# Optimization experiments

Measured on AMD Instinct MI355X. Metric: run time of the kernel, lower is better.

## Reference

```python
import jax, jax.numpy as jnp
import numpy as np

EPSILON = 1e-15
CUTOFF = 5.0
N_RBF = 16           # num_radial_filters -> RBF dim = 2*16+1 = 33
SCALE = 8            # _quadrature_points_per_atom_scaling


def poly_envelope_5_2(x):
    # e3nn.poly_envelope(5, 2): f'(x) ~ x^5 (1-x)^2, f(0)=1, f(1)=0
    x2 = x * x
    x6 = x2 * x2 * x2
    f = 1.0 - 28.0 * x6 + 48.0 * x6 * x - 21.0 * x6 * x2
    return jnp.where(x < 1.0, f, jnp.zeros_like(x))


def sin_cos_basis(r, n_rbf):
    r = r[..., None]                                  # [A,T,1]
    k = jnp.arange(1, n_rbf + 1, dtype=r.dtype)       # [n_rbf]
    return jnp.sqrt(2.0) * jnp.concatenate(
        [0.1 * jnp.ones_like(r), jnp.sin(k * jnp.pi * r), jnp.cos(k * jnp.pi * r)],
        axis=-1,
    )                                                 # [A,T,2*n_rbf+1]


def spherical_harmonics_l012_norm(d):
    # Real spherical harmonics up to l=2, e3nn m-ordering, normalization='norm'
    # (each l-block has unit norm for unit input directions).
    x, y, z = d[..., 0], d[..., 1], d[..., 2]
    r2 = x * x + y * y + z * z
    s3 = jnp.sqrt(3.0)
    one = jnp.ones_like(x)
    return jnp.stack(
        [
            one,                       # l=0
            y, z, x,                   # l=1 (m=-1,0,1)
            s3 * x * y,                # l=2 m=-2
            s3 * y * z,                # l=2 m=-1
            0.5 * (3.0 * z * z - r2),  # l=2 m=0
            s3 * x * z,                # l=2 m=1
            0.5 * s3 * (x * x - y * y) # l=2 m=2
        ],
        axis=-1,
    )                                  # [A,T,9]


def setup_inputs() -> dict:
    key = jax.random.key(0)
    k1, k2, k3, k4 = jax.random.split(key, 4)
    A, N = 64, 200000
    nuc_pos = 4.0 * jax.random.normal(k1, (A, 3), dtype=jnp.float32)
    grid_coords = 4.0 * jax.random.normal(k2, (N, 3), dtype=jnp.float32)
    weights = jax.random.uniform(k3, (N,), dtype=jnp.float32)
    n = jax.random.uniform(k4, (N,), dtype=jnp.float32)
    atom_mask = jnp.ones((A,), dtype=bool)
    return {"nuc_pos": nuc_pos, "atom_mask": atom_mask,
            "grid_coords": grid_coords, "weights": weights, "n": n}


def reference(nuc_pos, atom_mask, grid_coords, weights, n):
    g = grid_coords / CUTOFF                          # [N,3]
    p = nuc_pos / CUTOFF                              # [A,3]
    diff = p[:, None] - g[None]                       # [A,N,3]
    dist = jnp.linalg.norm(diff, axis=-1)             # [A,N]
    A, N = dist.shape
    T = min(N, SCALE * N // A)                        # static
    idx = jnp.argsort(dist, axis=1)[:, :T]            # [A,T] nearest grid points
    diff = jnp.take_along_axis(diff, idx[:, :, None], axis=1)   # [A,T,3]
    dist = jnp.take_along_axis(dist, idx, axis=1)                # [A,T]
    n_t = n[idx]                                      # [A,T]
    w_t = weights[idx]                                # [A,T]
    rbf = sin_cos_basis(dist, N_RBF) * poly_envelope_5_2(dist)[..., None]  # [A,T,33]
    dirs = diff / (dist[..., None] + EPSILON)         # [A,T,3]
    sh = spherical_harmonics_l012_norm(dirs)          # [A,T,9]
    node_feats = jnp.einsum('atr,ath,at,at->arh', rbf, sh, n_t, w_t)  # [A,33,9]
    return node_feats
```

## Files before the change

kernel.cpp:

```cpp
#include <hip/hip_runtime.h>


typedef float f32x4 __attribute__((ext_vector_type(4)));
typedef int   i32x4 __attribute__((ext_vector_type(4)));

#define SLICES 16
#define HBINS  8192
#define NB1    256
#define CLAMP0 4000u
#define CHA    4
#define CHF    4
#define NCHUNK (SLICES * CHA)
#define PBSTR  304
#define CUT25  0x41C80000u

__device__ __forceinline__ unsigned d2bits(float px, float py, float pz,
                                           float gx, float gy, float gz) {
  float dx = px - gx, dy = py - gy, dz = pz - gz;
  float d2 = __fmaf_rn(dx, dx, __fmaf_rn(dy, dy, __fmul_rn(dz, dz)));
  return __float_as_uint(d2);
}

__device__ __forceinline__ unsigned short tobf(float v) {
  return (unsigned short)((__float_as_uint(v) + 0x8000u) >> 16);
}

__device__ __forceinline__ void mfma_acc(f32x4& d, i32x4 a, i32x4 b) {
  asm("v_mfma_f32_16x16x32_bf16 %0, %1, %2, %0" : "+v"(d) : "v"(a), "v"(b));
}

__global__ __launch_bounds__(256) void enc_hist_store(
    const float* __restrict__ nuc, const float* __restrict__ grid, int N,
    unsigned* __restrict__ hists, unsigned* __restrict__ cnt,
    uint2* __restrict__ pairs, int scap, unsigned* __restrict__ ghist2) {
  __shared__ unsigned lh[NB1];
  __shared__ unsigned s_cnt;
  int a = blockIdx.x / SLICES, s = blockIdx.x % SLICES;
  int tid = threadIdx.x, lane = tid & 63;
  if (tid < NB1) lh[tid] = 0;
  if (tid == 0) s_cnt = 0;
  {
    const int stripe = HBINS / SLICES;
    unsigned* g2 = ghist2 + (size_t)a * HBINS + s * stripe;
    for (int t = tid; t < stripe; t += 256) g2[t] = 0;
  }
  __syncthreads();

  float px = nuc[3*a+0], py = nuc[3*a+1], pz = nuc[3*a+2];
  uint2* seg = pairs + (size_t)blockIdx.x * scap;
  const float4* G4 = (const float4*)grid;
  int nq = N >> 2;
  int qper = (nq + SLICES - 1) / SLICES;
  int qlo = s * qper, qhi = min(nq, qlo + qper);

  for (int qi = qlo + tid; qi < qhi; qi += 256) {
    float4 A4 = G4[3*qi], B4 = G4[3*qi+1], C4 = G4[3*qi+2];
    float xs[4] = {A4.x, A4.w, B4.z, C4.y};
    float ys[4] = {A4.y, B4.x, B4.w, C4.z};
    float zs[4] = {A4.z, B4.y, C4.x, C4.w};
    unsigned bt[4];
    #pragma unroll
    for (int k = 0; k < 4; ++k) {
      bt[k] = d2bits(px, py, pz, xs[k], ys[k], zs[k]);
      if (bt[k] < CUT25) {
        int cb = (int)(bt[k] >> 18) - (int)CLAMP0;
        atomicAdd(&lh[cb > 0 ? cb : 0], 1u);
      }
    }
    #pragma unroll
    for (int k = 0; k < 4; ++k) {
      bool sel = bt[k] < CUT25;
      unsigned long long mm = __ballot(sel);
      if (mm) {
        int leader = __ffsll(mm) - 1;
        unsigned base = 0;
        if (lane == leader) base = atomicAdd(&s_cnt, (unsigned)__popcll(mm));
        base = __shfl(base, leader);
        if (sel) {
          unsigned pos = base + (unsigned)__popcll(mm & ((1ull << lane) - 1ull));
          if (pos < (unsigned)scap) seg[pos] = make_uint2(bt[k], (unsigned)(4*qi + k));
        }
      }
    }
  }
  if (s == SLICES - 1) {
    for (int i = 4*nq + tid; i < N; i += 256) {
      unsigned bits = d2bits(px, py, pz, grid[3*i+0], grid[3*i+1], grid[3*i+2]);
      bool sel = bits < CUT25;
      if (sel) {
        int cb = (int)(bits >> 18) - (int)CLAMP0;
        atomicAdd(&lh[cb > 0 ? cb : 0], 1u);
      }
      unsigned long long mm = __ballot(sel);
      if (mm) {
        int leader = __ffsll(mm) - 1;
        unsigned base = 0;
        if (lane == leader) base = atomicAdd(&s_cnt, (unsigned)__popcll(mm));
        base = __shfl(base, leader);
        if (sel) {
          unsigned pos = base + (unsigned)__popcll(mm & ((1ull << lane) - 1ull));
          if (pos < (unsigned)scap) seg[pos] = make_uint2(bits, (unsigned)i);
        }
      }
    }
  }
  __syncthreads();
  if (tid < NB1) hists[(size_t)blockIdx.x * NB1 + tid] = lh[tid];
  if (tid == 0) cnt[blockIdx.x] = s_cnt;
}

__global__ __launch_bounds__(256) void enc_scan1(
    const unsigned* __restrict__ hists, unsigned T,
    unsigned* __restrict__ b1r, unsigned* __restrict__ r2r) {
  __shared__ unsigned lh[NB1];
  __shared__ unsigned s_bin, s_pre;
  int a = blockIdx.x, tid = threadIdx.x;
  if (tid < NB1) {
    unsigned acc = 0;
    const unsigned* base = hists + (size_t)a * SLICES * NB1 + tid;
    #pragma unroll
    for (int s = 0; s < SLICES; ++s) acc += base[(size_t)s * NB1];
    lh[tid] = acc;
  }
  if (tid == 0) { s_bin = NB1 - 1; s_pre = 0; }
  __syncthreads();
  if (tid < 64) {
    int lane = tid, base = 4 * lane;
    unsigned h0 = lh[base], h1 = lh[base+1], h2 = lh[base+2], h3 = lh[base+3];
    unsigned ssum = h0 + h1 + h2 + h3;
    unsigned p = ssum;
    #pragma unroll
    for (int d = 1; d < 64; d <<= 1) {
      unsigned t = __shfl_up(p, d);
      if (lane >= d) p += t;
    }
    unsigned excl = p - ssum;
    if (excl < T && T <= p) {
      unsigned cum = excl;
      unsigned hh[4] = {h0, h1, h2, h3};
      #pragma unroll
      for (int k = 0; k < 4; ++k) {
        if (cum + hh[k] >= T) { s_bin = (unsigned)(base + k); s_pre = cum; break; }
        cum += hh[k];
      }
    }
  }
  __syncthreads();
  if (tid == 0) { b1r[a] = s_bin; r2r[a] = T - s_pre; }
}

__global__ __launch_bounds__(256) void enc_fine(
    const unsigned* __restrict__ b1r, const unsigned* __restrict__ cnt,
    const uint2* __restrict__ pairs, int scap, unsigned* __restrict__ ghist2) {
  int seg_id = blockIdx.x / CHF, c = blockIdx.x % CHF;
  int a = seg_id / SLICES;
  unsigned b1c = b1r[a];
  unsigned tb1 = b1c + CLAMP0;
  int total = min((int)cnt[seg_id], scap);
  const uint2* seg = pairs + (size_t)seg_id * scap;
  unsigned* gh2 = ghist2 + (size_t)a * HBINS;
  for (int i = c * 256 + threadIdx.x; i < total; i += CHF * 256) {
    uint2 p = seg[i];
    unsigned cb = p.x >> 18;
    bool match = b1c ? (cb == tb1) : (cb <= CLAMP0);
    if (match) atomicAdd(&gh2[(p.x >> 5) & (HBINS - 1)], 1u);
  }
}

__global__ __launch_bounds__(256) void enc_scan2(
    const unsigned* __restrict__ ghist2, const unsigned* __restrict__ b1r,
    const unsigned* __restrict__ r2r, unsigned* __restrict__ thr) {
  __shared__ unsigned lh[HBINS];
  __shared__ unsigned s_bin, s_pre;
  int a = blockIdx.x, tid = threadIdx.x;
  const i32x4* gh = (const i32x4*)(ghist2 + (size_t)a * HBINS);
  for (int t = tid; t < HBINS / 4; t += 256) ((i32x4*)lh)[t] = gh[t];
  if (tid == 0) { s_bin = HBINS - 1; s_pre = 0; }
  __syncthreads();
  unsigned R = r2r[a];
  if (tid < 64) {
    int lane = tid;
    const int per = HBINS >> 6;
    int base = lane * per;
    unsigned ssum = 0;
    #pragma unroll 8
    for (int k = 0; k < per; ++k) ssum += lh[base + k];
    unsigned p = ssum;
    #pragma unroll
    for (int d = 1; d < 64; d <<= 1) {
      unsigned t = __shfl_up(p, d);
      if (lane >= d) p += t;
    }
    unsigned excl = p - ssum;
    unsigned long long mask = __ballot(excl < R && R <= p);
    if (mask) {
      int cl = (int)(__ffsll(mask) - 1);
      unsigned excl_cl = __shfl(excl, cl);
      unsigned Rp = R - excl_cl;
      int b2 = cl * per + 2 * lane;
      unsigned h0 = lh[b2], h1 = lh[b2 + 1];
      unsigned ss2 = h0 + h1;
      unsigned p2 = ss2;
      #pragma unroll
      for (int d = 1; d < 64; d <<= 1) {
        unsigned t = __shfl_up(p2, d);
        if (lane >= d) p2 += t;
      }
      unsigned excl2 = p2 - ss2;
      if (excl2 < Rp && Rp <= p2) {
        if (excl2 + h0 >= Rp) s_bin = (unsigned)b2;
        else                  s_bin = (unsigned)(b2 + 1);
      }
    }
  }
  __syncthreads();
  if (tid == 0) thr[a] = ((b1r[a] + CLAMP0) << 13) | s_bin;
}

__global__ __launch_bounds__(256, 4) void enc_accum(
    const float* __restrict__ nuc, const float* __restrict__ grid,
    const float* __restrict__ wv, const float* __restrict__ nv,
    const unsigned* __restrict__ thrv, const unsigned* __restrict__ cnt,
    const uint2* __restrict__ pairs, int scap, float* __restrict__ pb) {
  __shared__ __align__(16) unsigned short lds[4][4608];
  int seg_id = blockIdx.x / CHA, c = blockIdx.x % CHA;
  int a = seg_id / SLICES;
  int tid = threadIdx.x, lane = tid & 63, w = tid >> 6;
  unsigned short* SB = &lds[w][0];

  {
    i32x4 z = {0, 0, 0, 0};
    i32x4* zp = (i32x4*)SB;
    #pragma unroll
    for (int t = 0; t < 9; ++t) zp[lane + t * 64] = z;
  }

  unsigned thr = thrv[a];
  float px = nuc[3*a+0], py = nuc[3*a+1], pz = nuc[3*a+2];
  int total = min((int)cnt[seg_id], scap);
  const uint2* lst = pairs + (size_t)seg_id * scap;

  f32x4 acc0 = {0,0,0,0}, acc1 = {0,0,0,0}, acc2 = {0,0,0,0};
  int m = lane & 15, q = lane >> 4;
  const float SQRT2 = 1.41421356237309515f;
  const float PIF   = 3.14159265358979323846f;
  const float S3    = 1.73205080756887729f;

  for (int jb = c * 256 + w * 64; jb < total; jb += CHA * 256) {
    int j = jb + lane;
    bool valid = j < total;
    uint2 pr = valid ? lst[j] : make_uint2(0xFFFFFFFFu, 0u);
    bool live = valid && ((pr.x >> 5) <= thr);
    unsigned gi = pr.y;
    if (live) {
      float gx = grid[3*gi+0], gy = grid[3*gi+1], gz = grid[3*gi+2];
      float dx = px - gx, dy = py - gy, dz = pz - gz;
      float d2 = __fmaf_rn(dx, dx, __fmaf_rn(dy, dy, dz * dz));
#if __has_builtin(__builtin_amdgcn_sqrtf)
      float rn = __builtin_amdgcn_sqrtf(d2) * 0.2f;
#else
      float rn = sqrtf(d2) * 0.2f;
#endif
      float x2 = rn * rn;
      float x6 = x2 * x2 * x2;
      float e  = __fmaf_rn(x6, __fmaf_rn(-21.f, x2, __fmaf_rn(48.f, rn, -28.f)), 1.f);
      float f  = SQRT2 * e;
      float nw = nv[gi] * wv[gi];
#if __has_builtin(__builtin_amdgcn_rcpf)
      float inv = 0.2f * __builtin_amdgcn_rcpf(rn + 1e-15f);
#else
      float inv = 0.2f / (rn + 1e-15f);
#endif
      float X = dx * inv, Y = dy * inv, Z = dz * inv;
      float r2 = __fmaf_rn(X, X, __fmaf_rn(Y, Y, Z * Z));
      SB[3456 + 0*72 + lane] = tobf(nw);
      SB[3456 + 1*72 + lane] = tobf(nw * Y);
      SB[3456 + 2*72 + lane] = tobf(nw * Z);
      SB[3456 + 3*72 + lane] = tobf(nw * X);
      SB[3456 + 4*72 + lane] = tobf(nw * S3 * X * Y);
      SB[3456 + 5*72 + lane] = tobf(nw * S3 * Y * Z);
      SB[3456 + 6*72 + lane] = tobf(nw * 0.5f * __fmaf_rn(3.f, Z * Z, -r2));
      SB[3456 + 7*72 + lane] = tobf(nw * S3 * X * Z);
      SB[3456 + 8*72 + lane] = tobf(nw * 0.5f * S3 * (X * X - Y * Y));
      float s1 = __sinf(PIF * rn), c1 = __cosf(PIF * rn);
      SB[0 * 72 + lane]  = tobf(0.1f * f);
      float sk = s1, ck = c1;
      SB[1 * 72 + lane]  = tobf(f * sk);
      SB[17 * 72 + lane] = tobf(f * ck);
      #pragma unroll
      for (int k = 2; k <= 16; ++k) {
        float sn = __fmaf_rn(sk, c1, ck * s1);
        float cn = __fmaf_rn(ck, c1, -(sk * s1));
        sk = sn; ck = cn;
        SB[k * 72 + lane]        = tobf(f * sk);
        SB[(16 + k) * 72 + lane] = tobf(f * ck);
      }
    } else {
      #pragma unroll
      for (int h = 0; h < 9; ++h) SB[3456 + h * 72 + lane] = 0;
    }
    #pragma unroll
    for (int g = 0; g < 2; ++g) {
      int cb = 8 * q + 32 * g;
      i32x4 bf = *(const i32x4*)&SB[3456 + m * 72 + cb];
      i32x4 a0 = *(const i32x4*)&SB[(0  + m) * 72 + cb];
      mfma_acc(acc0, a0, bf);
      i32x4 a1 = *(const i32x4*)&SB[(16 + m) * 72 + cb];
      mfma_acc(acc1, a1, bf);
      i32x4 a2 = *(const i32x4*)&SB[(32 + m) * 72 + cb];
      mfma_acc(acc2, a2, bf);
    }
  }
  asm volatile("s_nop 7\n\ts_nop 7" : "+v"(acc0), "+v"(acc1), "+v"(acc2));

  float* redw = (float*)&lds[w][0];
  if (m < 9) {
    #pragma unroll
    for (int t = 0; t < 4; ++t) {
      int row = 4 * q + t;
      redw[(row +  0) * 9 + m] = acc0[t];
      redw[(row + 16) * 9 + m] = acc1[t];
      if (row + 32 < 33) redw[(row + 32) * 9 + m] = acc2[t];
    }
  }
  __syncthreads();
  float* pbb = pb + (size_t)blockIdx.x * PBSTR;
  for (int v = tid; v < 297; v += 256) {
    float s0 = ((const float*)&lds[0][0])[v] + ((const float*)&lds[1][0])[v];
    float s1 = ((const float*)&lds[2][0])[v] + ((const float*)&lds[3][0])[v];
    pbb[v] = s0 + s1;
  }
}

__global__ __launch_bounds__(256) void enc_reduce(
    const float* __restrict__ pb, float* __restrict__ out, int nout) {
  int idx = blockIdx.x * 256 + threadIdx.x;
  if (idx >= nout) return;
  int a = idx / 297, v = idx - a * 297;
  const float* p = pb + (size_t)a * NCHUNK * PBSTR + v;
  float s = 0.f;
  #pragma unroll 8
  for (int k = 0; k < NCHUNK; ++k) s += p[(size_t)k * PBSTR];
  out[idx] = s;
}

extern "C" void kernel_launch(void* const* d_in, const int* in_sizes, int n_in,
                              void* d_out, int out_size, void* d_ws, size_t ws_size,
                              hipStream_t stream) {
  const float* nuc  = (const float*)d_in[0];
  const float* grid = (const float*)d_in[2];
  const float* wts  = (const float*)d_in[3];
  const float* nn   = (const float*)d_in[4];
  int A = in_sizes[0] / 3;
  int N = in_sizes[2] / 3;
  long long t8 = (8LL * (long long)N) / (long long)A;
  unsigned T = (unsigned)(t8 < (long long)N ? t8 : (long long)N);

  unsigned* ws     = (unsigned*)d_ws;
  unsigned* cnt    = ws;
  unsigned* b1r    = cnt + A * SLICES;
  unsigned* r2r    = b1r + A;
  unsigned* thr    = r2r + A;
  unsigned* hists  = thr + A;
  unsigned* ghist2 = hists + (size_t)A * SLICES * NB1;
  float*    pb     = (float*)(ghist2 + (size_t)A * HBINS);
  uint2*    pairs  = (uint2*)(pb + (size_t)A * SLICES * CHA * PBSTR);

  int SCAP = (N + SLICES - 1) / SLICES;
  {
    long long head  = (long long)(((unsigned*)pairs) - ws);
    long long avail = (long long)(ws_size / 4) - head;
    long long need  = 2LL * SCAP * A * SLICES;
    if (avail > 0 && need > avail) SCAP = (int)(avail / (2LL * A * SLICES));
  }
  float* out = (float*)d_out;
  int nout = A * 297;

  enc_hist_store<<<A * SLICES,         256, 0, stream>>>(nuc, grid, N, hists, cnt,
                                                         pairs, SCAP, ghist2);
  enc_scan1     <<<A,                  256, 0, stream>>>(hists, T, b1r, r2r);
  enc_fine      <<<A * SLICES * CHF,   256, 0, stream>>>(b1r, cnt, pairs, SCAP, ghist2);
  enc_scan2     <<<A,                  256, 0, stream>>>(ghist2, b1r, r2r, thr);
  enc_accum     <<<A * SLICES * CHA,   256, 0, stream>>>(nuc, grid, wts, nn, thr, cnt,
                                                         pairs, SCAP, pb);
  enc_reduce    <<<(nout + 255) / 256, 256, 0, stream>>>(pb, out, nout);
}
```

Measured before the change: 66.58 us.

## Fold histogram scans into neighbouring kernels and shrink fine histogram to 512 bins

Removes the two standalone scan kernels. Each enc_fine block now recomputes the coarse-bin prefix scan itself. Each enc_accum block loads a per-atom 512-bin fine histogram and finds the threshold bin locally. This cuts two kernel launches and the large 8192-bin zeroing and scan traffic, at the cost of redundant per-block scan work and a coarser threshold quantization (bits 9+ instead of 5+), which may admit slightly more near-tie points than the exact top-T set.

```diff
diff --git a/kernel.cpp b/kernel.cpp
--- a/kernel.cpp
+++ b/kernel.cpp
@@ -5,11 +5,11 @@
 typedef int   i32x4 __attribute__((ext_vector_type(4)));
 
 #define SLICES 16
-#define HBINS  8192
 #define NB1    256
+#define NB2    512
 #define CLAMP0 4000u
 #define CHA    4
-#define CHF    4
+#define CHF    2
 #define NCHUNK (SLICES * CHA)
 #define PBSTR  304
 #define CUT25  0x41C80000u
@@ -40,9 +40,8 @@
   if (tid < NB1) lh[tid] = 0;
   if (tid == 0) s_cnt = 0;
   {
-    const int stripe = HBINS / SLICES;
-    unsigned* g2 = ghist2 + (size_t)a * HBINS + s * stripe;
-    for (int t = tid; t < stripe; t += 256) g2[t] = 0;
+    const int stripe = NB2 / SLICES;
+    if (tid < stripe) ghist2[(size_t)a * NB2 + s * stripe + tid] = 0;
   }
   __syncthreads();
 
@@ -109,17 +108,21 @@
   if (tid == 0) cnt[blockIdx.x] = s_cnt;
 }
 
-__global__ __launch_bounds__(256) void enc_scan1(
-    const unsigned* __restrict__ hists, unsigned T,
-    unsigned* __restrict__ b1r, unsigned* __restrict__ r2r) {
+__global__ __launch_bounds__(256) void enc_fine(
+    const unsigned* __restrict__ hists, const unsigned* __restrict__ cnt,
+    const uint2* __restrict__ pairs, int scap, unsigned T,
+    unsigned* __restrict__ b1r, unsigned* __restrict__ r2r,
+    unsigned* __restrict__ ghist2) {
   __shared__ unsigned lh[NB1];
   __shared__ unsigned s_bin, s_pre;
-  int a = blockIdx.x, tid = threadIdx.x;
+  int seg_id = blockIdx.x / CHF, c = blockIdx.x % CHF;
+  int a = seg_id / SLICES, s = seg_id % SLICES;
+  int tid = threadIdx.x;
   if (tid < NB1) {
     unsigned acc = 0;
     const unsigned* base = hists + (size_t)a * SLICES * NB1 + tid;
     #pragma unroll
-    for (int s = 0; s < SLICES; ++s) acc += base[(size_t)s * NB1];
+    for (int t = 0; t < SLICES; ++t) acc += base[(size_t)t * NB1];
     lh[tid] = acc;
   }
   if (tid == 0) { s_bin = NB1 - 1; s_pre = 0; }
@@ -146,83 +149,30 @@
     }
   }
   __syncthreads();
-  if (tid == 0) { b1r[a] = s_bin; r2r[a] = T - s_pre; }
-}
-
-__global__ __launch_bounds__(256) void enc_fine(
-    const unsigned* __restrict__ b1r, const unsigned* __restrict__ cnt,
-    const uint2* __restrict__ pairs, int scap, unsigned* __restrict__ ghist2) {
-  int seg_id = blockIdx.x / CHF, c = blockIdx.x % CHF;
-  int a = seg_id / SLICES;
-  unsigned b1c = b1r[a];
+  unsigned b1c = s_bin;
+  if (s == 0 && c == 0 && tid == 0) { b1r[a] = s_bin; r2r[a] = T - s_pre; }
+
   unsigned tb1 = b1c + CLAMP0;
   int total = min((int)cnt[seg_id], scap);
   const uint2* seg = pairs + (size_t)seg_id * scap;
-  unsigned* gh2 = ghist2 + (size_t)a * HBINS;
-  for (int i = c * 256 + threadIdx.x; i < total; i += CHF * 256) {
+  unsigned* gh2 = ghist2 + (size_t)a * NB2;
+  for (int i = c * 256 + tid; i < total; i += CHF * 256) {
     uint2 p = seg[i];
     unsigned cb = p.x >> 18;
     bool match = b1c ? (cb == tb1) : (cb <= CLAMP0);
-    if (match) atomicAdd(&gh2[(p.x >> 5) & (HBINS - 1)], 1u);
-  }
-}
-
-__global__ __launch_bounds__(256) void enc_scan2(
-    const unsigned* __restrict__ ghist2, const unsigned* __restrict__ b1r,
-    const unsigned* __restrict__ r2r, unsigned* __restrict__ thr) {
-  __shared__ unsigned lh[HBINS];
-  __shared__ unsigned s_bin, s_pre;
-  int a = blockIdx.x, tid = threadIdx.x;
-  const i32x4* gh = (const i32x4*)(ghist2 + (size_t)a * HBINS);
-  for (int t = tid; t < HBINS / 4; t += 256) ((i32x4*)lh)[t] = gh[t];
-  if (tid == 0) { s_bin = HBINS - 1; s_pre = 0; }
-  __syncthreads();
-  unsigned R = r2r[a];
-  if (tid < 64) {
-    int lane = tid;
-    const int per = HBINS >> 6;
-    int base = lane * per;
-    unsigned ssum = 0;
-    #pragma unroll 8
-    for (int k = 0; k < per; ++k) ssum += lh[base + k];
-    unsigned p = ssum;
-    #pragma unroll
-    for (int d = 1; d < 64; d <<= 1) {
-      unsigned t = __shfl_up(p, d);
-      if (lane >= d) p += t;
-    }
-    unsigned excl = p - ssum;
-    unsigned long long mask = __ballot(excl < R && R <= p);
-    if (mask) {
-      int cl = (int)(__ffsll(mask) - 1);
-      unsigned excl_cl = __shfl(excl, cl);
-      unsigned Rp = R - excl_cl;
-      int b2 = cl * per + 2 * lane;
-      unsigned h0 = lh[b2], h1 = lh[b2 + 1];
-      unsigned ss2 = h0 + h1;
-      unsigned p2 = ss2;
-      #pragma unroll
-      for (int d = 1; d < 64; d <<= 1) {
-        unsigned t = __shfl_up(p2, d);
-        if (lane >= d) p2 += t;
-      }
-      unsigned excl2 = p2 - ss2;
-      if (excl2 < Rp && Rp <= p2) {
-        if (excl2 + h0 >= Rp) s_bin = (unsigned)b2;
-        else                  s_bin = (unsigned)(b2 + 1);
-      }
-    }
-  }
-  __syncthreads();
-  if (tid == 0) thr[a] = ((b1r[a] + CLAMP0) << 13) | s_bin;
+    if (match) atomicAdd(&gh2[(p.x >> 9) & (NB2 - 1)], 1u);
+  }
 }
 
 __global__ __launch_bounds__(256, 4) void enc_accum(
     const float* __restrict__ nuc, const float* __restrict__ grid,
     const float* __restrict__ wv, const float* __restrict__ nv,
-    const unsigned* __restrict__ thrv, const unsigned* __restrict__ cnt,
+    const unsigned* __restrict__ b1r, const unsigned* __restrict__ r2r,
+    const unsigned* __restrict__ ghist2, const unsigned* __restrict__ cnt,
     const uint2* __restrict__ pairs, int scap, float* __restrict__ pb) {
   __shared__ __align__(16) unsigned short lds[4][4608];
+  __shared__ unsigned lh2[NB2];
+  __shared__ unsigned s_bin2;
   int seg_id = blockIdx.x / CHA, c = blockIdx.x % CHA;
   int a = seg_id / SLICES;
   int tid = threadIdx.x, lane = tid & 63, w = tid >> 6;
@@ -234,8 +184,38 @@
     #pragma unroll
     for (int t = 0; t < 9; ++t) zp[lane + t * 64] = z;
   }
-
-  unsigned thr = thrv[a];
+  {
+    const unsigned* gh2 = ghist2 + (size_t)a * NB2;
+    lh2[tid] = gh2[tid];
+    lh2[tid + 256] = gh2[tid + 256];
+  }
+  if (tid == 0) s_bin2 = NB2 - 1;
+  __syncthreads();
+  unsigned R = r2r[a];
+  if (tid < 64) {
+    int lane2 = tid, base = 8 * lane2;
+    unsigned hh[8], ssum = 0;
+    #pragma unroll
+    for (int k = 0; k < 8; ++k) { hh[k] = lh2[base + k]; ssum += hh[k]; }
+    unsigned p = ssum;
+    #pragma unroll
+    for (int d = 1; d < 64; d <<= 1) {
+      unsigned t = __shfl_up(p, d);
+      if (lane2 >= d) p += t;
+    }
+    unsigned excl = p - ssum;
+    if (excl < R && R <= p) {
+      unsigned cum = excl;
+      #pragma unroll
+      for (int k = 0; k < 8; ++k) {
+        if (cum + hh[k] >= R) { s_bin2 = (unsigned)(base + k); break; }
+        cum += hh[k];
+      }
+    }
+  }
+  __syncthreads();
+  unsigned thr = ((b1r[a] + CLAMP0) << 9) | s_bin2;
+
   float px = nuc[3*a+0], py = nuc[3*a+1], pz = nuc[3*a+2];
   int total = min((int)cnt[seg_id], scap);
   const uint2* lst = pairs + (size_t)seg_id * scap;
@@ -250,7 +230,7 @@
     int j = jb + lane;
     bool valid = j < total;
     uint2 pr = valid ? lst[j] : make_uint2(0xFFFFFFFFu, 0u);
-    bool live = valid && ((pr.x >> 5) <= thr);
+    bool live = valid && ((pr.x >> 9) <= thr);
     unsigned gi = pr.y;
     if (live) {
       float gx = grid[3*gi+0], gy = grid[3*gi+1], gz = grid[3*gi+2];
@@ -360,10 +340,9 @@
   unsigned* cnt    = ws;
   unsigned* b1r    = cnt + A * SLICES;
   unsigned* r2r    = b1r + A;
-  unsigned* thr    = r2r + A;
-  unsigned* hists  = thr + A;
+  unsigned* hists  = r2r + A;
   unsigned* ghist2 = hists + (size_t)A * SLICES * NB1;
-  float*    pb     = (float*)(ghist2 + (size_t)A * HBINS);
+  float*    pb     = (float*)(ghist2 + (size_t)A * NB2);
   uint2*    pairs  = (uint2*)(pb + (size_t)A * SLICES * CHA * PBSTR);
 
   int SCAP = (N + SLICES - 1) / SLICES;
@@ -378,10 +357,9 @@
 
   enc_hist_store<<<A * SLICES,         256, 0, stream>>>(nuc, grid, N, hists, cnt,
                                                          pairs, SCAP, ghist2);
-  enc_scan1     <<<A,                  256, 0, stream>>>(hists, T, b1r, r2r);
-  enc_fine      <<<A * SLICES * CHF,   256, 0, stream>>>(b1r, cnt, pairs, SCAP, ghist2);
-  enc_scan2     <<<A,                  256, 0, stream>>>(ghist2, b1r, r2r, thr);
-  enc_accum     <<<A * SLICES * CHA,   256, 0, stream>>>(nuc, grid, wts, nn, thr, cnt,
-                                                         pairs, SCAP, pb);
+  enc_fine      <<<A * SLICES * CHF,   256, 0, stream>>>(hists, cnt, pairs, SCAP, T,
+                                                         b1r, r2r, ghist2);
+  enc_accum     <<<A * SLICES * CHA,   256, 0, stream>>>(nuc, grid, wts, nn, b1r, r2r,
+                                                         ghist2, cnt, pairs, SCAP, pb);
   enc_reduce    <<<(nout + 255) / 256, 256, 0, stream>>>(pb, out, nout);
 }
```

Measured after the change: 65.48 us. No clear change (-1.7%).
